# Performance work log

Measured on AMD Instinct MI355X. Metric: run time of the kernel, lower is better.

## Reference

```python
import jax, jax.numpy as jnp
import numpy as np

H = 1024      # hidden_size
V = 32000     # output_size (vocab)
L = 512       # max_length (encoder positions)
B = 256       # batch


def setup_inputs() -> dict:
    key = jax.random.key(0)
    ks = jax.random.split(key, 12)
    s = 0.02
    return {
        "input": jax.random.randint(ks[0], (B,), 0, V),
        "hidden": jax.random.normal(ks[1], (1, B, H), jnp.float32),
        "encoder_outputs": jax.random.normal(ks[2], (L, H), jnp.float32),
        # learned params (PyTorch layout: Linear weight is [out, in])
        "emb": jax.random.normal(ks[3], (V, H), jnp.float32) * s,
        "attn_W": jax.random.normal(ks[4], (L, 2 * H), jnp.float32) * s,
        "attn_b": jnp.zeros((L,), jnp.float32),
        "comb_W": jax.random.normal(ks[5], (H, 2 * H), jnp.float32) * s,
        "comb_b": jnp.zeros((H,), jnp.float32),
        "W_ih": jax.random.normal(ks[6], (3 * H, H), jnp.float32) * s,
        "W_hh": jax.random.normal(ks[7], (3 * H, H), jnp.float32) * s,
        "b_ih": jnp.zeros((3 * H,), jnp.float32),
        "b_hh": jnp.zeros((3 * H,), jnp.float32),
        "out_W": jax.random.normal(ks[8], (V, H), jnp.float32) * s,
        "out_b": jnp.zeros((V,), jnp.float32),
    }


def reference(input, hidden, encoder_outputs, emb, attn_W, attn_b,
              comb_W, comb_b, W_ih, W_hh, b_ih, b_hh, out_W, out_b):
    h = hidden[0]                                   # [B,H]
    embedded = emb[input]                           # [B,H] (dropout in eval mode = identity)
    attn_logits = jnp.concatenate([embedded, h], axis=1) @ attn_W.T + attn_b
    attn_weights = jax.nn.softmax(attn_logits, axis=1)        # [B,L]
    attn_applied = attn_weights @ encoder_outputs              # [B,H]
    x = jnp.concatenate([embedded, attn_applied], axis=1) @ comb_W.T + comb_b
    x = jax.nn.relu(x)                                         # [B,H]
    # single-step GRU (PyTorch gate layout: r, z, n)
    gi = x @ W_ih.T + b_ih                                     # [B,3H]
    gh = h @ W_hh.T + b_hh                                     # [B,3H]
    gi_r, gi_z, gi_n = jnp.split(gi, 3, axis=1)
    gh_r, gh_z, gh_n = jnp.split(gh, 3, axis=1)
    r = jax.nn.sigmoid(gi_r + gh_r)
    z = jax.nn.sigmoid(gi_z + gh_z)
    n = jnp.tanh(gi_n + r * gh_n)
    h_new = (1.0 - z) * n + z * h                              # [B,H]
    output = jax.nn.log_softmax(h_new @ out_W.T + out_b, axis=1)  # [B,V]
    return output, h_new[None], attn_weights
```

## Files before the change

### kernel.cpp

```cpp
#include <hip/hip_runtime.h>
#include <hip/hip_bf16.h>
#include <cstdint>

#define DEVI __device__ __forceinline__

typedef __bf16 bf16x8 __attribute__((ext_vector_type(8)));
typedef float  f32x4  __attribute__((ext_vector_type(4)));

constexpr int Hdim = 1024;
constexpr int Vdim = 32000;
constexpr int Ldim = 512;
constexpr int Bdim = 256;

DEVI unsigned short f2bf(float f) {
  __bf16 h = (__bf16)f;
  return __builtin_bit_cast(unsigned short, h);
}

constexpr int FP4 = 36;
constexpr int GF_GRID = Vdim / 128;

__global__ __launch_bounds__(1024, 4)
void gemm_flat8(const unsigned short* __restrict__ A,
                const float* __restrict__ W,
                const float* __restrict__ bias,
                float* __restrict__ C,
                float2* __restrict__ plse)
{
  __shared__ unsigned short lW[4][128 * FP4];

  const int t    = threadIdx.x;
  const int lane = t & 63;
  const int wv   = t >> 6;
  const int r16  = lane & 15;
  const int k8   = (lane >> 4) * 8;
  const int n0   = blockIdx.x * 128;

  const int srow = t >> 3;
  const int stc  = (t & 7) * 4;

  const float*          Wb = W + (size_t)(n0 + srow) * 1024 + stc;
  const unsigned short* Ab = A + (size_t)(wv * 16 + r16) * 1024 + k8;

  f32x4 acc[8];
#pragma unroll
  for (int n = 0; n < 8; ++n)
#pragma unroll
    for (int r = 0; r < 4; ++r) acc[n][r] = 0.f;

  f32x4 w0_, w1_;
  uint4 a0_, a1_, a2_, a3_;

#define LOADW(RW, KT) RW = *reinterpret_cast<const f32x4*>(Wb + (KT) * 32)
#define LOADA(RA, KT) RA = *reinterpret_cast<const uint4*>(Ab + (KT) * 32)

#define STOREW(RW, BUF) do {                                                   \
    ushort4 u_;                                                                \
    u_.x = f2bf(RW[0]); u_.y = f2bf(RW[1]);                                    \
    u_.z = f2bf(RW[2]); u_.w = f2bf(RW[3]);                                    \
    *reinterpret_cast<ushort4*>(&lW[BUF][srow * FP4 + stc]) = u_;              \
  } while (0)

#define COMP(RA, BUF) do {                                                     \
    _Pragma("unroll")                                                          \
    for (int n = 0; n < 8; ++n) {                                              \
      bf16x8 bw_ = *reinterpret_cast<const bf16x8*>(                           \
          &lW[BUF][(n * 16 + r16) * FP4 + k8]);                                \
      acc[n] = __builtin_amdgcn_mfma_f32_16x16x32_bf16(                        \
          __builtin_bit_cast(bf16x8, RA), bw_, acc[n], 0, 0, 0);               \
    }                                                                          \
  } while (0)

#define GFBAR() do {                                                           \
    asm volatile("s_waitcnt lgkmcnt(0)" ::: "memory");                         \
    __builtin_amdgcn_sched_barrier(0);                                         \
    __builtin_amdgcn_s_barrier();                                              \
    __builtin_amdgcn_sched_barrier(0);                                         \
  } while (0)

  LOADW(w0_, 0); LOADW(w1_, 1);
  LOADA(a0_, 0); LOADA(a1_, 1); LOADA(a2_, 2); LOADA(a3_, 3);
  STOREW(w0_, 0); LOADW(w0_, 2);
  STOREW(w1_, 1); LOADW(w1_, 3);
  GFBAR();

  for (int kt = 0; kt < 32; kt += 4) {
    COMP(a0_, 0);
    STOREW(w0_, 2);
    { const int kn = (kt + 4 < 32) ? kt + 4 : 31; LOADW(w0_, kn); LOADA(a0_, kn); }
    GFBAR();

    COMP(a1_, 1);
    STOREW(w1_, 3);
    { const int kn = (kt + 5 < 32) ? kt + 5 : 31; LOADW(w1_, kn); LOADA(a1_, kn); }
    GFBAR();

    COMP(a2_, 2);
    STOREW(w0_, 0);
    { const int kn = (kt + 6 < 32) ? kt + 6 : 31; LOADW(w0_, kn); LOADA(a2_, kn); }
    GFBAR();

    COMP(a3_, 3);
    STOREW(w1_, 1);
    { const int kn = (kt + 7 < 32) ? kt + 7 : 31; LOADW(w1_, kn); LOADA(a3_, kn); }
    GFBAR();
  }

#undef GFBAR
#undef COMP
#undef STOREW
#undef LOADA
#undef LOADW

#pragma unroll
  for (int n = 0; n < 8; ++n) {
    const int col = n0 + n * 16 + r16;
    const float bv = bias[col];
    const int rbase = wv * 16 + (lane >> 4) * 4;
#pragma unroll
    for (int r = 0; r < 4; ++r) {
      const float v = acc[n][r] + bv;
      acc[n][r] = v;
      C[(size_t)(rbase + r) * Vdim + col] = v;
    }
  }
#pragma unroll
  for (int r = 0; r < 4; ++r) {
    float mx = -1e30f;
#pragma unroll
    for (int n = 0; n < 8; ++n) mx = fmaxf(mx, acc[n][r]);
#pragma unroll
    for (int o = 1; o < 16; o <<= 1) mx = fmaxf(mx, __shfl_xor(mx, o, 16));
    float s = 0.f;
#pragma unroll
    for (int n = 0; n < 8; ++n) s += __expf(acc[n][r] - mx);
#pragma unroll
    for (int o = 1; o < 16; o <<= 1) s += __shfl_xor(s, o, 16);
    if (r16 == 0) {
      const int row = wv * 16 + (lane >> 4) * 4 + r;
      plse[(size_t)row * gridDim.x + blockIdx.x] = make_float2(mx, s);
    }
  }
}

struct GP {
  const float* A; const float* W; float* C;
  int K, ldc, ldb, col_off, aact, nsplit, gx;
};

template<bool BTRANS>
__global__ __launch_bounds__(256, 2)
void gemm_multi(GP q0, GP q1, int n0blk)
{
  constexpr int MT = 128, PITCH = 40, ITA = 4, MR = 2;

  __shared__ unsigned short lA[2 * MT * PITCH];
  __shared__ unsigned short lW[2 * 64 * PITCH];

  GP p = q0;
  int id = blockIdx.x;
  if (id >= n0blk) { p = q1; id -= n0blk; }
  const int bx  = id % p.gx;
  const int rem = id / p.gx;
  const int by  = rem & 1;
  const int kz  = rem >> 1;

  const int m0 = by * MT;
  const int n0 = bx * 64;
  const int NK = p.K / (32 * p.nsplit);
  const int kb = kz * NK;

  const int t  = threadIdx.x;
  const int tr = t >> 3;
  const int tc = (t & 7) * 4;

  const float* Af = p.A + (size_t)m0 * p.K;

  const int lane = t & 63;
  const int wv   = t >> 6;
  const int r16  = lane & 15;
  const int k8   = (lane >> 4) * 8;

  f32x4 acc[MR][4];
#pragma unroll
  for (int m = 0; m < MR; ++m)
#pragma unroll
    for (int n = 0; n < 4; ++n)
#pragma unroll
      for (int r = 0; r < 4; ++r) acc[m][n][r] = 0.f;

  struct RS { f32x4 ra[ITA]; f32x4 rw[2]; };

  auto loadT = [&](RS& rg, int kt) {
    const int ko = (kb + kt) * 32;
#pragma unroll
    for (int i = 0; i < ITA; ++i)
      rg.ra[i] = *reinterpret_cast<const f32x4*>(
          Af + (size_t)(tr + 32 * i) * p.K + ko + tc);
    if constexpr (BTRANS) {
      const float* wp = p.W + (size_t)(ko + tr) * p.ldb + n0 + (t & 7) * 8;
      rg.rw[0] = *reinterpret_cast<const f32x4*>(wp);
      rg.rw[1] = *reinterpret_cast<const f32x4*>(wp + 4);
    } else {
#pragma unroll
      for (int i = 0; i < 2; ++i)
        rg.rw[i] = *reinterpret_cast<const f32x4*>(
            p.W + (size_t)(n0 + tr + 32 * i) * p.ldb + ko + tc);
    }
  };

  auto storeT = [&](RS& rg, int bo) {
    unsigned short* sA = &lA[bo * MT * PITCH];
    unsigned short* sW = &lW[bo * 64 * PITCH];
#pragma unroll
    for (int i = 0; i < ITA; ++i) {
      f32x4 v = rg.ra[i];
      if (p.aact) { v[0]=fmaxf(v[0],0.f); v[1]=fmaxf(v[1],0.f);
                    v[2]=fmaxf(v[2],0.f); v[3]=fmaxf(v[3],0.f); }
      ushort4 u;
      u.x = f2bf(v[0]); u.y = f2bf(v[1]); u.z = f2bf(v[2]); u.w = f2bf(v[3]);
      *reinterpret_cast<ushort4*>(&sA[(tr + 32 * i) * PITCH + tc]) = u;
    }
    if constexpr (BTRANS) {
      const int hb = (t & 7) * 8;
#pragma unroll
      for (int j = 0; j < 4; ++j) {
        sW[(hb + j)     * PITCH + tr] = f2bf(rg.rw[0][j]);
        sW[(hb + 4 + j) * PITCH + tr] = f2bf(rg.rw[1][j]);
      }
    } else {
#pragma unroll
      for (int i = 0; i < 2; ++i) {
        f32x4 v = rg.rw[i]; ushort4 u;
        u.x = f2bf(v[0]); u.y = f2bf(v[1]); u.z = f2bf(v[2]); u.w = f2bf(v[3]);
        *reinterpret_cast<ushort4*>(&sW[(tr + 32 * i) * PITCH + tc]) = u;
      }
    }
  };

  auto comp = [&](int bo) {
    const unsigned short* sA = &lA[bo * MT * PITCH];
    const unsigned short* sW = &lW[bo * 64 * PITCH];
    bf16x8 af[MR], bfr[4];
#pragma unroll
    for (int m = 0; m < MR; ++m)
      af[m] = *reinterpret_cast<const bf16x8*>(&sA[(wv * 32 + m * 16 + r16) * PITCH + k8]);
#pragma unroll
    for (int n = 0; n < 4; ++n)
      bfr[n] = *reinterpret_cast<const bf16x8*>(&sW[(n * 16 + r16) * PITCH + k8]);
#pragma unroll
    for (int m = 0; m < MR; ++m)
#pragma unroll
      for (int n = 0; n < 4; ++n)
        acc[m][n] = __builtin_amdgcn_mfma_f32_16x16x32_bf16(af[m], bfr[n], acc[m][n], 0, 0, 0);
  };

#define GB_BARRIER() do { \
    asm volatile("s_waitcnt lgkmcnt(0)" ::: "memory"); \
    __builtin_amdgcn_sched_barrier(0); \
    __builtin_amdgcn_s_barrier(); \
  } while (0)

  RS ra_, rb_;
  loadT(ra_, 0);
  loadT(rb_, 1);
  storeT(ra_, 0);
  GB_BARRIER();

  for (int kt = 0; kt < NK; kt += 2) {
    if (kt + 2 < NK) loadT(ra_, kt + 2);
    comp(0);
    storeT(rb_, 1);
    GB_BARRIER();
    if (kt + 3 < NK) loadT(rb_, kt + 3);
    comp(1);
    if (kt + 2 < NK) {
      storeT(ra_, 0);
      GB_BARRIER();
    }
  }
#undef GB_BARRIER

#pragma unroll
  for (int n = 0; n < 4; ++n) {
    const int col = n0 + n * 16 + r16;
#pragma unroll
    for (int m = 0; m < MR; ++m) {
      const int rbase = m0 + wv * 32 + m * 16 + (lane >> 4) * 4;
#pragma unroll
      for (int r = 0; r < 4; ++r)
        atomicAdd(&p.C[(size_t)(rbase + r) * p.ldc + p.col_off + col],
                  acc[m][n][r]);
    }
  }
}

__global__ void prep_kernel(const int* __restrict__ ids, const float* __restrict__ hid,
                            const float* __restrict__ emb,
                            const float* __restrict__ attn_b, const float* __restrict__ comb_b,
                            const float* __restrict__ b_ih, const float* __restrict__ b_hh,
                            float* __restrict__ X0, float* __restrict__ X1,
                            float* __restrict__ alog, float* __restrict__ xact,
                            float* __restrict__ gi, float* __restrict__ gh)
{
  const int b = blockIdx.x, t = threadIdx.x;
  const int row = ids[b];
  f32x4 e = *reinterpret_cast<const f32x4*>(emb + (size_t)row * Hdim + t * 4);
  *reinterpret_cast<f32x4*>(X0 + (size_t)b * 2048 + t * 4) = e;
  *reinterpret_cast<f32x4*>(X1 + (size_t)b * 2048 + t * 4) = e;
  f32x4 h = *reinterpret_cast<const f32x4*>(hid + (size_t)b * Hdim + t * 4);
  *reinterpret_cast<f32x4*>(X0 + (size_t)b * 2048 + 1024 + t * 4) = h;
  f32x4 z4 = {0.f, 0.f, 0.f, 0.f};
  *reinterpret_cast<f32x4*>(X1 + (size_t)b * 2048 + 1024 + t * 4) = z4;
  if (t < 128)
    *reinterpret_cast<f32x4*>(alog + (size_t)b * Ldim + t * 4) =
        *reinterpret_cast<const f32x4*>(attn_b + t * 4);
  *reinterpret_cast<f32x4*>(xact + (size_t)b * Hdim + t * 4) =
      *reinterpret_cast<const f32x4*>(comb_b + t * 4);
#pragma unroll
  for (int i = 0; i < 3; ++i) {
    *reinterpret_cast<f32x4*>(gi + (size_t)b * 3072 + i * 1024 + t * 4) =
        *reinterpret_cast<const f32x4*>(b_ih + i * 1024 + t * 4);
    *reinterpret_cast<f32x4*>(gh + (size_t)b * 3072 + i * 1024 + t * 4) =
        *reinterpret_cast<const f32x4*>(b_hh + i * 1024 + t * 4);
  }
}

__global__ void attn_softmax_kernel(const float* __restrict__ logits, float* __restrict__ wout)
{
  __shared__ float red[256];
  const int b = blockIdx.x, t = threadIdx.x;
  const float x0 = logits[b * Ldim + t];
  const float x1 = logits[b * Ldim + 256 + t];
  red[t] = fmaxf(x0, x1); __syncthreads();
  for (int o = 128; o > 0; o >>= 1) { if (t < o) red[t] = fmaxf(red[t], red[t + o]); __syncthreads(); }
  const float m = red[0]; __syncthreads();
  const float e0 = __expf(x0 - m), e1 = __expf(x1 - m);
  red[t] = e0 + e1; __syncthreads();
  for (int o = 128; o > 0; o >>= 1) { if (t < o) red[t] += red[t + o]; __syncthreads(); }
  const float inv = 1.f / red[0];
  wout[b * Ldim + t]       = e0 * inv;
  wout[b * Ldim + 256 + t] = e1 * inv;
}

DEVI float sigm(float x) { return 1.f / (1.f + __expf(-x)); }

__global__ void gru_kernel(const float* __restrict__ gi, const float* __restrict__ gh,
                           const float* __restrict__ hin,
                           float* __restrict__ hnew, unsigned short* __restrict__ hnbf)
{
  const int idx = blockIdx.x * 256 + threadIdx.x;
  const int b = idx >> 10, j = idx & 1023;
  const float* gib = gi + (size_t)b * 3072;
  const float* ghb = gh + (size_t)b * 3072;
  const float r = sigm(gib[j] + ghb[j]);
  const float z = sigm(gib[1024 + j] + ghb[1024 + j]);
  const float n = tanhf(gib[2048 + j] + r * ghb[2048 + j]);
  const float h = hin[idx];
  const float hn = (1.f - z) * n + z * h;
  hnew[idx] = hn;
  hnbf[idx] = f2bf(hn);
}

__global__ void lsm_sub2(const float2* __restrict__ part, int npart,
                         float* __restrict__ out)
{
  __shared__ float rm[256], rs[256];
  const int b = blockIdx.x >> 3, c = blockIdx.x & 7;
  const int t = threadIdx.x;
  float m = -1e30f, s = 0.f;
  for (int j = t; j < npart; j += 256) {
    const float2 p = part[(size_t)b * npart + j];
    const float nm = fmaxf(m, p.x);
    s = s * __expf(m - nm) + p.y * __expf(p.x - nm);
    m = nm;
  }
  rm[t] = m; rs[t] = s; __syncthreads();
  for (int o = 128; o > 0; o >>= 1) {
    if (t < o) {
      const float m2 = rm[t + o], s2 = rs[t + o];
      const float nm = fmaxf(rm[t], m2);
      rs[t] = rs[t] * __expf(rm[t] - nm) + s2 * __expf(m2 - nm);
      rm[t] = nm;
    }
    __syncthreads();
  }
  const float lse = rm[0] + __logf(rs[0]);
  f32x4* row4 = reinterpret_cast<f32x4*>(out + (size_t)b * Vdim) + c * 1000;
  for (int i = t; i < 1000; i += 256) {
    f32x4 x = row4[i];
    x[0] -= lse; x[1] -= lse; x[2] -= lse; x[3] -= lse;
    row4[i] = x;
  }
}

extern "C" void kernel_launch(void* const* d_in, const int* in_sizes, int n_in,
                              void* d_out, int out_size, void* d_ws, size_t ws_size,
                              hipStream_t stream)
{
  (void)in_sizes; (void)n_in; (void)out_size; (void)ws_size;

  const int*   ids    = (const int*)  d_in[0];
  const float* hid    = (const float*)d_in[1];
  const float* enc    = (const float*)d_in[2];
  const float* emb    = (const float*)d_in[3];
  const float* attn_W = (const float*)d_in[4];
  const float* attn_b = (const float*)d_in[5];
  const float* comb_W = (const float*)d_in[6];
  const float* comb_b = (const float*)d_in[7];
  const float* W_ih   = (const float*)d_in[8];
  const float* W_hh   = (const float*)d_in[9];
  const float* b_ih   = (const float*)d_in[10];
  const float* b_hh   = (const float*)d_in[11];
  const float* out_W  = (const float*)d_in[12];
  const float* out_b  = (const float*)d_in[13];

  float* out_logits = (float*)d_out;
  float* out_h      = out_logits + (size_t)Bdim * Vdim;
  float* out_attw   = out_h + (size_t)Bdim * Hdim;

  char* w = (char*)d_ws;
  float* X0   = (float*)w; w += (size_t)Bdim * 2048 * 4;
  float* X1   = (float*)w; w += (size_t)Bdim * 2048 * 4;
  float* alog = (float*)w; w += (size_t)Bdim * Ldim * 4;
  float* xact = (float*)w; w += (size_t)Bdim * Hdim * 4;
  float* gi   = (float*)w; w += (size_t)Bdim * 3 * Hdim * 4;
  float* gh   = (float*)w; w += (size_t)Bdim * 3 * Hdim * 4;
  unsigned short* hnbf = (unsigned short*)w; w += (size_t)Bdim * Hdim * 2;
  float2* plse = (float2*)w; w += (size_t)Bdim * GF_GRID * 8;

  prep_kernel<<<Bdim, 256, 0, stream>>>(ids, hid, emb, attn_b, comb_b, b_ih, b_hh,
                                        X0, X1, alog, xact, gi, gh);

  {
    GP p0 = { X0,  attn_W, alog, 2048, Ldim,     2048, 0, 0, 8,  Ldim / 64 };
    GP p1 = { hid, W_hh,   gh,   1024, 3 * Hdim, 1024, 0, 0, 4,  3 * Hdim / 64 };
    const int n0blk = p0.gx * 2 * p0.nsplit;
    const int nblk  = n0blk + p1.gx * 2 * p1.nsplit;
    gemm_multi<false><<<nblk, 256, 0, stream>>>(p0, p1, n0blk);
  }

  attn_softmax_kernel<<<Bdim, 256, 0, stream>>>(alog, out_attw);

  {
    GP p0 = { out_attw, enc, X1, 512, 2048, Hdim, 1024, 0, 4, Hdim / 64 };
    const int nblk = p0.gx * 2 * p0.nsplit;
    gemm_multi<true><<<nblk, 256, 0, stream>>>(p0, p0, nblk);
  }

  {
    GP p0 = { X1, comb_W, xact, 2048, Hdim, 2048, 0, 0, 8, Hdim / 64 };
    const int nblk = p0.gx * 2 * p0.nsplit;
    gemm_multi<false><<<nblk, 256, 0, stream>>>(p0, p0, nblk);
  }

  {
    GP p0 = { xact, W_ih, gi, 1024, 3 * Hdim, 1024, 0, 1, 4, 3 * Hdim / 64 };
    const int nblk = p0.gx * 2 * p0.nsplit;
    gemm_multi<false><<<nblk, 256, 0, stream>>>(p0, p0, nblk);
  }

  gru_kernel<<<Bdim * Hdim / 256, 256, 0, stream>>>(gi, gh, hid, out_h, hnbf);

  gemm_flat8<<<GF_GRID, 1024, 0, stream>>>(hnbf, out_W, out_b, out_logits, plse);

  lsm_sub2<<<Bdim * 8, 256, 0, stream>>>(plse, GF_GRID, out_logits);
}
```

Baseline: 123.3 us.

## Restage output-projection GEMM with 256-wide K chunks and double-buffered LDS

The vocab projection GEMM now stages 256-wide K slices of out_W (converted to bf16) into two large LDS buffers instead of 32-wide slices in four small buffers. The loop drops from 32 barrier-separated steps to 4, with each step issuing 64 MFMAs while the next chunk's global loads are in flight. The aim is fewer barriers and more loads in flight per thread. In exchange it needs far more registers and LDS (about 135 KB per block, launch bounds reduced to one block per CU), which lowers occupancy and shortens the pipeline.

Result: slower. 134.9 us (+9.4%).

```diff
diff --git a/kernel.cpp b/kernel.cpp
--- a/kernel.cpp
+++ b/kernel.cpp
@@ -17,57 +17,69 @@
   return __builtin_bit_cast(unsigned short, h);
 }
 
-constexpr int FP4 = 36;
+constexpr int QP = 264;
 constexpr int GF_GRID = Vdim / 128;
 
-__global__ __launch_bounds__(1024, 4)
-void gemm_flat8(const unsigned short* __restrict__ A,
+__global__ __launch_bounds__(1024, 1)
+void gemm_flat9(const unsigned short* __restrict__ A,
                 const float* __restrict__ W,
                 const float* __restrict__ bias,
                 float* __restrict__ C,
                 float2* __restrict__ plse)
 {
-  __shared__ unsigned short lW[4][128 * FP4];
+  __shared__ unsigned short lWq[2][128 * QP];
 
   const int t    = threadIdx.x;
   const int lane = t & 63;
   const int wv   = t >> 6;
   const int r16  = lane & 15;
-  const int k8   = (lane >> 4) * 8;
+  const int kq   = lane >> 4;
   const int n0   = blockIdx.x * 128;
 
-  const int srow = t >> 3;
-  const int stc  = (t & 7) * 4;
-
-  const float*          Wb = W + (size_t)(n0 + srow) * 1024 + stc;
-  const unsigned short* Ab = A + (size_t)(wv * 16 + r16) * 1024 + k8;
-
   f32x4 acc[8];
 #pragma unroll
   for (int n = 0; n < 8; ++n)
 #pragma unroll
     for (int r = 0; r < 4; ++r) acc[n][r] = 0.f;
 
-  f32x4 w0_, w1_;
-  uint4 a0_, a1_, a2_, a3_;
-
-#define LOADW(RW, KT) RW = *reinterpret_cast<const f32x4*>(Wb + (KT) * 32)
-#define LOADA(RA, KT) RA = *reinterpret_cast<const uint4*>(Ab + (KT) * 32)
-
-#define STOREW(RW, BUF) do {                                                   \
-    ushort4 u_;                                                                \
-    u_.x = f2bf(RW[0]); u_.y = f2bf(RW[1]);                                    \
-    u_.z = f2bf(RW[2]); u_.w = f2bf(RW[3]);                                    \
-    *reinterpret_cast<ushort4*>(&lW[BUF][srow * FP4 + stc]) = u_;              \
-  } while (0)
-
-#define COMP(RA, BUF) do {                                                     \
+  f32x4 wr[8];
+  uint4 aA[8], aB[8];
+
+#define WLOADQ(Q) do {                                                         \
     _Pragma("unroll")                                                          \
-    for (int n = 0; n < 8; ++n) {                                              \
-      bf16x8 bw_ = *reinterpret_cast<const bf16x8*>(                           \
-          &lW[BUF][(n * 16 + r16) * FP4 + k8]);                                \
-      acc[n] = __builtin_amdgcn_mfma_f32_16x16x32_bf16(                        \
-          __builtin_bit_cast(bf16x8, RA), bw_, acc[n], 0, 0, 0);               \
+    for (int j = 0; j < 8; ++j)                                                \
+      wr[j] = *reinterpret_cast<const f32x4*>(                                 \
+          W + (size_t)(n0 + wv * 8 + j) * 1024 + (Q) * 256 + lane * 4);        \
+  } while (0)
+
+#define WSTOREQ(BUF) do {                                                      \
+    _Pragma("unroll")                                                          \
+    for (int j = 0; j < 8; ++j) {                                              \
+      ushort4 u_;                                                              \
+      u_.x = f2bf(wr[j][0]); u_.y = f2bf(wr[j][1]);                            \
+      u_.z = f2bf(wr[j][2]); u_.w = f2bf(wr[j][3]);                            \
+      *reinterpret_cast<ushort4*>(                                             \
+          &lWq[BUF][(wv * 8 + j) * QP + lane * 4]) = u_;                       \
+    }                                                                          \
+  } while (0)
+
+#define ALOADQ(AR, Q) do {                                                     \
+    _Pragma("unroll")                                                          \
+    for (int j = 0; j < 8; ++j)                                                \
+      AR[j] = *reinterpret_cast<const uint4*>(                                 \
+          A + (size_t)(wv * 16 + r16) * 1024 + (Q) * 256 + j * 32 + kq * 8);   \
+  } while (0)
+
+#define COMPQ(AR, BUF) do {                                                    \
+    _Pragma("unroll")                                                          \
+    for (int j = 0; j < 8; ++j) {                                              \
+      _Pragma("unroll")                                                        \
+      for (int n = 0; n < 8; ++n) {                                            \
+        bf16x8 bw_ = *reinterpret_cast<const bf16x8*>(                         \
+            &lWq[BUF][(n * 16 + r16) * QP + j * 32 + kq * 8]);                 \
+        acc[n] = __builtin_amdgcn_mfma_f32_16x16x32_bf16(                      \
+            __builtin_bit_cast(bf16x8, AR[j]), bw_, acc[n], 0, 0, 0);          \
+      }                                                                        \
     }                                                                          \
   } while (0)
 
@@ -78,45 +90,39 @@
     __builtin_amdgcn_sched_barrier(0);                                         \
   } while (0)
 
-  LOADW(w0_, 0); LOADW(w1_, 1);
-  LOADA(a0_, 0); LOADA(a1_, 1); LOADA(a2_, 2); LOADA(a3_, 3);
-  STOREW(w0_, 0); LOADW(w0_, 2);
-  STOREW(w1_, 1); LOADW(w1_, 3);
+  WLOADQ(0);
+  WSTOREQ(0);
+  ALOADQ(aA, 0);
   GFBAR();
 
-  for (int kt = 0; kt < 32; kt += 4) {
-    COMP(a0_, 0);
-    STOREW(w0_, 2);
-    { const int kn = (kt + 4 < 32) ? kt + 4 : 31; LOADW(w0_, kn); LOADA(a0_, kn); }
-    GFBAR();
-
-    COMP(a1_, 1);
-    STOREW(w1_, 3);
-    { const int kn = (kt + 5 < 32) ? kt + 5 : 31; LOADW(w1_, kn); LOADA(a1_, kn); }
-    GFBAR();
-
-    COMP(a2_, 2);
-    STOREW(w0_, 0);
-    { const int kn = (kt + 6 < 32) ? kt + 6 : 31; LOADW(w0_, kn); LOADA(a2_, kn); }
-    GFBAR();
-
-    COMP(a3_, 3);
-    STOREW(w1_, 1);
-    { const int kn = (kt + 7 < 32) ? kt + 7 : 31; LOADW(w1_, kn); LOADA(a3_, kn); }
-    GFBAR();
-  }
+  WLOADQ(1); ALOADQ(aB, 1);
+  COMPQ(aA, 0);
+  WSTOREQ(1);
+  GFBAR();
+
+  WLOADQ(2); ALOADQ(aA, 2);
+  COMPQ(aB, 1);
+  WSTOREQ(0);
+  GFBAR();
+
+  WLOADQ(3); ALOADQ(aB, 3);
+  COMPQ(aA, 0);
+  WSTOREQ(1);
+  GFBAR();
+
+  COMPQ(aB, 1);
 
 #undef GFBAR
-#undef COMP
-#undef STOREW
-#undef LOADA
-#undef LOADW
+#undef COMPQ
+#undef ALOADQ
+#undef WSTOREQ
+#undef WLOADQ
 
 #pragma unroll
   for (int n = 0; n < 8; ++n) {
     const int col = n0 + n * 16 + r16;
     const float bv = bias[col];
-    const int rbase = wv * 16 + (lane >> 4) * 4;
+    const int rbase = wv * 16 + kq * 4;
 #pragma unroll
     for (int r = 0; r < 4; ++r) {
       const float v = acc[n][r] + bv;
@@ -137,7 +143,7 @@
 #pragma unroll
     for (int o = 1; o < 16; o <<= 1) s += __shfl_xor(s, o, 16);
     if (r16 == 0) {
-      const int row = wv * 16 + (lane >> 4) * 4 + r;
+      const int row = wv * 16 + kq * 4 + r;
       plse[(size_t)row * gridDim.x + blockIdx.x] = make_float2(mx, s);
     }
   }
@@ -462,7 +468,7 @@
 
   gru_kernel<<<Bdim * Hdim / 256, 256, 0, stream>>>(gi, gh, hid, out_h, hnbf);
 
-  gemm_flat8<<<GF_GRID, 1024, 0, stream>>>(hnbf, out_W, out_b, out_logits, plse);
+  gemm_flat9<<<GF_GRID, 1024, 0, stream>>>(hnbf, out_W, out_b, out_logits, plse);
 
   lsm_sub2<<<Bdim * 8, 256, 0, stream>>>(plse, GF_GRID, out_logits);
 }
```

## Stream output-projection weights straight into LDS with direct global-to-LDS loads

Applied to the files above, without the earlier changes.

The vocab projection GEMM no longer stages fp32 weights through registers and converts them to bf16 before the LDS store. It now uses global_load_lds to copy fp32 tiles directly into an XOR-swizzled LDS buffer, with a 3-deep ring and vmcnt-based waits replacing lgkmcnt waits. The bf16 conversion moves to the LDS read side. This frees registers and VALU work in the load path, but doubles LDS footprint and bandwidth per tile and adds conversion inside the compute loop.

Result: slower. 128.6 us (+4.3%).

```diff
diff --git a/kernel.cpp b/kernel.cpp
--- a/kernel.cpp
+++ b/kernel.cpp
@@ -17,29 +17,36 @@
   return __builtin_bit_cast(unsigned short, h);
 }
 
-constexpr int FP4 = 36;
+DEVI void load_lds16(const void* g, void* l) {
+  __builtin_amdgcn_global_load_lds(
+      (const __attribute__((address_space(1))) unsigned int*)g,
+      (__attribute__((address_space(3))) unsigned int*)l, 16, 0, 0);
+}
+
 constexpr int GF_GRID = Vdim / 128;
 
 __global__ __launch_bounds__(1024, 4)
-void gemm_flat8(const unsigned short* __restrict__ A,
-                const float* __restrict__ W,
-                const float* __restrict__ bias,
-                float* __restrict__ C,
-                float2* __restrict__ plse)
-{
-  __shared__ unsigned short lW[4][128 * FP4];
+void gemm_flat10(const unsigned short* __restrict__ A,
+                 const float* __restrict__ W,
+                 const float* __restrict__ bias,
+                 float* __restrict__ C,
+                 float2* __restrict__ plse)
+{
+  __shared__ float lW4[4][128 * 32];
 
   const int t    = threadIdx.x;
   const int lane = t & 63;
   const int wv   = t >> 6;
   const int r16  = lane & 15;
-  const int k8   = (lane >> 4) * 8;
+  const int kq   = lane >> 4;
+  const int k8   = kq * 8;
   const int n0   = blockIdx.x * 128;
 
-  const int srow = t >> 3;
-  const int stc  = (t & 7) * 4;
-
-  const float*          Wb = W + (size_t)(n0 + srow) * 1024 + stc;
+  const int srow  = t >> 3;
+  const int sslot = t & 7;
+
+  const float* Wsrc = W + (size_t)(n0 + srow) * 1024
+                        + ((sslot ^ (srow & 7)) * 4);
   const unsigned short* Ab = A + (size_t)(wv * 16 + r16) * 1024 + k8;
 
   f32x4 acc[8];
@@ -48,75 +55,62 @@
 #pragma unroll
     for (int r = 0; r < 4; ++r) acc[n][r] = 0.f;
 
-  f32x4 w0_, w1_;
   uint4 a0_, a1_, a2_, a3_;
 
-#define LOADW(RW, KT) RW = *reinterpret_cast<const f32x4*>(Wb + (KT) * 32)
-#define LOADA(RA, KT) RA = *reinterpret_cast<const uint4*>(Ab + (KT) * 32)
-
-#define STOREW(RW, BUF) do {                                                   \
-    ushort4 u_;                                                                \
-    u_.x = f2bf(RW[0]); u_.y = f2bf(RW[1]);                                    \
-    u_.z = f2bf(RW[2]); u_.w = f2bf(RW[3]);                                    \
-    *reinterpret_cast<ushort4*>(&lW[BUF][srow * FP4 + stc]) = u_;              \
+#define ISSUE(BUF, ASET, KT) do {                                              \
+    load_lds16(Wsrc + (KT) * 32, lW4[BUF] + wv * 256);                         \
+    ASET = *reinterpret_cast<const uint4*>(Ab + (KT) * 32);                    \
   } while (0)
 
 #define COMP(RA, BUF) do {                                                     \
     _Pragma("unroll")                                                          \
     for (int n = 0; n < 8; ++n) {                                              \
-      bf16x8 bw_ = *reinterpret_cast<const bf16x8*>(                           \
-          &lW[BUF][(n * 16 + r16) * FP4 + k8]);                                \
+      const int row_ = n * 16 + r16;                                           \
+      const float* rb_ = lW4[BUF] + row_ * 32;                                 \
+      const int sw_ = row_ & 7;                                                \
+      f32x4 wA = *reinterpret_cast<const f32x4*>(rb_ + (((kq*2)   ^ sw_)*4));  \
+      f32x4 wB = *reinterpret_cast<const f32x4*>(rb_ + (((kq*2+1) ^ sw_)*4));  \
+      bf16x8 v_;                                                               \
+      v_[0]=(__bf16)wA[0]; v_[1]=(__bf16)wA[1];                                \
+      v_[2]=(__bf16)wA[2]; v_[3]=(__bf16)wA[3];                                \
+      v_[4]=(__bf16)wB[0]; v_[5]=(__bf16)wB[1];                                \
+      v_[6]=(__bf16)wB[2]; v_[7]=(__bf16)wB[3];                                \
       acc[n] = __builtin_amdgcn_mfma_f32_16x16x32_bf16(                        \
-          __builtin_bit_cast(bf16x8, RA), bw_, acc[n], 0, 0, 0);               \
+          __builtin_bit_cast(bf16x8, RA), v_, acc[n], 0, 0, 0);                \
     }                                                                          \
   } while (0)
 
-#define GFBAR() do {                                                           \
-    asm volatile("s_waitcnt lgkmcnt(0)" ::: "memory");                         \
+#define STEP(P, I, ANEXT, ACUR) do {                                           \
+    asm volatile("s_waitcnt vmcnt(4)" ::: "memory");                           \
     __builtin_amdgcn_sched_barrier(0);                                         \
     __builtin_amdgcn_s_barrier();                                              \
     __builtin_amdgcn_sched_barrier(0);                                         \
+    { const int kn_ = ((I) + 3 < 32) ? (I) + 3 : 31;                           \
+      ISSUE(((P) + 3) & 3, ANEXT, kn_); }                                      \
+    __builtin_amdgcn_sched_barrier(0);                                         \
+    COMP(ACUR, P);                                                             \
   } while (0)
 
-  LOADW(w0_, 0); LOADW(w1_, 1);
-  LOADA(a0_, 0); LOADA(a1_, 1); LOADA(a2_, 2); LOADA(a3_, 3);
-  STOREW(w0_, 0); LOADW(w0_, 2);
-  STOREW(w1_, 1); LOADW(w1_, 3);
-  GFBAR();
+  ISSUE(0, a0_, 0);
+  ISSUE(1, a1_, 1);
+  ISSUE(2, a2_, 2);
 
   for (int kt = 0; kt < 32; kt += 4) {
-    COMP(a0_, 0);
-    STOREW(w0_, 2);
-    { const int kn = (kt + 4 < 32) ? kt + 4 : 31; LOADW(w0_, kn); LOADA(a0_, kn); }
-    GFBAR();
-
-    COMP(a1_, 1);
-    STOREW(w1_, 3);
-    { const int kn = (kt + 5 < 32) ? kt + 5 : 31; LOADW(w1_, kn); LOADA(a1_, kn); }
-    GFBAR();
-
-    COMP(a2_, 2);
-    STOREW(w0_, 0);
-    { const int kn = (kt + 6 < 32) ? kt + 6 : 31; LOADW(w0_, kn); LOADA(a2_, kn); }
-    GFBAR();
-
-    COMP(a3_, 3);
-    STOREW(w1_, 1);
-    { const int kn = (kt + 7 < 32) ? kt + 7 : 31; LOADW(w1_, kn); LOADA(a3_, kn); }
-    GFBAR();
-  }
-
-#undef GFBAR
+    STEP(0, kt,     a3_, a0_);
+    STEP(1, kt + 1, a0_, a1_);
+    STEP(2, kt + 2, a1_, a2_);
+    STEP(3, kt + 3, a2_, a3_);
+  }
+
+#undef STEP
 #undef COMP
-#undef STOREW
-#undef LOADA
-#undef LOADW
+#undef ISSUE
 
 #pragma unroll
   for (int n = 0; n < 8; ++n) {
     const int col = n0 + n * 16 + r16;
     const float bv = bias[col];
-    const int rbase = wv * 16 + (lane >> 4) * 4;
+    const int rbase = wv * 16 + kq * 4;
 #pragma unroll
     for (int r = 0; r < 4; ++r) {
       const float v = acc[n][r] + bv;
@@ -137,7 +131,7 @@
 #pragma unroll
     for (int o = 1; o < 16; o <<= 1) s += __shfl_xor(s, o, 16);
     if (r16 == 0) {
-      const int row = wv * 16 + (lane >> 4) * 4 + r;
+      const int row = wv * 16 + kq * 4 + r;
       plse[(size_t)row * gridDim.x + blockIdx.x] = make_float2(mx, s);
     }
   }
@@ -462,7 +456,7 @@
 
   gru_kernel<<<Bdim * Hdim / 256, 256, 0, stream>>>(gi, gh, hid, out_h, hnbf);
 
-  gemm_flat8<<<GF_GRID, 1024, 0, stream>>>(hnbf, out_W, out_b, out_logits, plse);
+  gemm_flat10<<<GF_GRID, 1024, 0, stream>>>(hnbf, out_W, out_b, out_logits, plse);
 
   lsm_sub2<<<Bdim * 8, 256, 0, stream>>>(plse, GF_GRID, out_logits);
 }
```
